# Optimization experiments

Hardware: AMD Instinct MI355X
Metric: run time of the kernel (lower is better)

The kernel has to match this reference:

```python
import jax, jax.numpy as jnp
import numpy as np

EMB_D, N_SLOTS, KEY_D, N_ITER = 768, 8, 128, 5
ATTN_EPS = 1e-8
LN_EPS = 1e-5


def layer_norm(x, g, b):
    mu = jnp.mean(x, axis=-1, keepdims=True)
    var = jnp.mean(jnp.square(x - mu), axis=-1, keepdims=True)
    return (x - mu) * jax.lax.rsqrt(var + LN_EPS) * g + b


def xavier(key, shape):
    fan_in, fan_out = shape[-1], shape[-2] if len(shape) > 1 else shape[-1]
    a = float(np.sqrt(6.0 / (fan_in + fan_out)))
    return jax.random.uniform(key, shape, jnp.float32, -a, a)


def setup_inputs() -> dict:
    key = jax.random.key(0)
    ks = jax.random.split(key, 24)
    B, N = 128, 196
    k = KEY_D
    inp = {
        "features": jax.random.normal(ks[0], (B, N, EMB_D), jnp.float32),
        "slot_noise": jax.random.normal(ks[1], (B, N_SLOTS, k), jnp.float32),
        # LayerNorms
        "ln_in_g": jnp.ones((EMB_D,), jnp.float32), "ln_in_b": jnp.zeros((EMB_D,), jnp.float32),
        "ln_slot_g": jnp.ones((k,), jnp.float32), "ln_slot_b": jnp.zeros((k,), jnp.float32),
        "ln_out_g": jnp.ones((k,), jnp.float32), "ln_out_b": jnp.zeros((k,), jnp.float32),
        "ln_dec_g": jnp.ones((k,), jnp.float32), "ln_dec_b": jnp.zeros((k,), jnp.float32),
        # slot prior
        "mu": xavier(ks[2], (1, 1, k)),
        "log_sigma": xavier(ks[3], (1, 1, k)),
        # projections (torch Linear weight layout: [out, in])
        "Wk": xavier(ks[4], (k, EMB_D)),
        "Wq": xavier(ks[5], (k, k)),
        "Wv": xavier(ks[6], (k, EMB_D)),
        # GRUCell
        "W_ih": jax.random.uniform(ks[7], (3 * k, k), jnp.float32, -1.0/np.sqrt(k), 1.0/np.sqrt(k)),
        "W_hh": jax.random.uniform(ks[8], (3 * k, k), jnp.float32, -1.0/np.sqrt(k), 1.0/np.sqrt(k)),
        "b_ih": jnp.zeros((3 * k,), jnp.float32),
        "b_hh": jnp.zeros((3 * k,), jnp.float32),
        # slot MLP
        "mlp_W1": xavier(ks[9], (k, k)), "mlp_b1": jnp.zeros((k,), jnp.float32),
        "mlp_W2": xavier(ks[10], (k, k)), "mlp_b2": jnp.zeros((k,), jnp.float32),
        # decoder
        "dec_W1": xavier(ks[11], (2 * k, k)), "dec_b1": jnp.zeros((2 * k,), jnp.float32),
        "dec_W2": xavier(ks[12], (EMB_D, 2 * k)), "dec_b2": jnp.zeros((EMB_D,), jnp.float32),
        "dec_W3": xavier(ks[13], (EMB_D, EMB_D)), "dec_b3": jnp.zeros((EMB_D,), jnp.float32),
    }
    return inp


def gru_cell(x, h, W_ih, W_hh, b_ih, b_hh):
    gi = x @ W_ih.T + b_ih  # [*, 3k]
    gh = h @ W_hh.T + b_hh
    ir, iz, inn = jnp.split(gi, 3, axis=-1)
    hr, hz, hn = jnp.split(gh, 3, axis=-1)
    r = jax.nn.sigmoid(ir + hr)
    z = jax.nn.sigmoid(iz + hz)
    n = jnp.tanh(inn + r * hn)
    return (1.0 - z) * n + z * h


def reference(features, slot_noise, ln_in_g, ln_in_b, ln_slot_g, ln_slot_b,
              ln_out_g, ln_out_b, ln_dec_g, ln_dec_b, mu, log_sigma,
              Wk, Wq, Wv, W_ih, W_hh, b_ih, b_hh,
              mlp_W1, mlp_b1, mlp_W2, mlp_b2,
              dec_W1, dec_b1, dec_W2, dec_b2, dec_W3, dec_b3):
    feats_ln = layer_norm(features, ln_in_g, ln_in_b)  # [B,N,E]
    slots = slot_noise * jnp.exp(log_sigma) + mu       # [B,K,D]
    k_proj = (feats_ln @ Wk.T) * (KEY_D ** -0.5)       # [B,N,D]
    v_proj = feats_ln @ Wv.T                           # [B,N,D]

    attn_vis = None
    for _ in range(N_ITER):
        slots_prev = slots
        s_ln = layer_norm(slots, ln_slot_g, ln_slot_b)
        q = s_ln @ Wq.T                                # [B,K,D]
        logits = jnp.einsum('bnd,bkd->bnk', k_proj, q)
        attn_vis = jax.nn.softmax(logits, axis=-1)     # softmax over slots
        attn = attn_vis + ATTN_EPS
        attn = attn / jnp.sum(attn, axis=-2, keepdims=True)  # normalize over tokens
        updates = jnp.einsum('bnk,bnd->bkd', attn, v_proj)
        slots = gru_cell(updates, slots_prev, W_ih, W_hh, b_ih, b_hh)
        h = jax.nn.relu(layer_norm(slots, ln_out_g, ln_out_b) @ mlp_W1.T + mlp_b1)
        slots = slots + (h @ mlp_W2.T + mlp_b2)

    sf = layer_norm(slots, ln_dec_g, ln_dec_b)
    sf = jax.nn.relu(sf @ dec_W1.T + dec_b1)
    sf = jax.nn.relu(sf @ dec_W2.T + dec_b2)
    sf = sf @ dec_W3.T + dec_b3                        # [B,K,E]
    recon = jnp.einsum('bkd,bnk->bnd', sf, attn_vis)   # [B,N,E]
    recon_loss = jnp.mean(jnp.square(recon - features))
    return slots, attn_vis, recon_loss
```

## Files before the change

kernel.cpp:

```cpp
#include <hip/hip_runtime.h>
#include <hip/hip_bf16.h>
#include <math.h>

#define B_    128
#define N_    196
#define E_    768
#define K_    8
#define D_    128
#define BNR   (B_*N_)
#define ITERS 5

#define OFF_PART   0
#define OFF_SDEC   512
#define OFF_WBF    66048
#define OFF_KPBF   639488
#define OFF_VPTBF  2343424
#define OFF_ABF    4178432

typedef __attribute__((ext_vector_type(8))) short bf16x8;
typedef __attribute__((ext_vector_type(4))) float f32x4;

#define MFMA16(a, b, c) __builtin_amdgcn_mfma_f32_16x16x32_bf16(a, b, c, 0, 0, 0)

__device__ __forceinline__ float wave_red_sum64(float v) {
    #pragma unroll
    for (int o = 32; o > 0; o >>= 1) v += __shfl_xor(v, o);
    return v;
}

__device__ __forceinline__ unsigned short f2bf(float v) {
    union { float f; unsigned int u; } c; c.f = v;
    unsigned int u = c.u + 0x7fffu + ((c.u >> 16) & 1u);
    return (unsigned short)(u >> 16);
}

__device__ __forceinline__ void gl_lds16(const void* g, void* l) {
    __builtin_amdgcn_global_load_lds(
        (const __attribute__((address_space(1))) unsigned int*)g,
        (__attribute__((address_space(3))) unsigned int*)l, 16, 0, 0);
}

__device__ __forceinline__ int swz128(int row, int j) {
    return row * 128 + ((((j >> 3) ^ (row & 7))) << 3) + (j & 7);
}
__device__ __forceinline__ int swz256(int row, int j) {
    return row * 256 + ((((j >> 3) ^ (row & 7))) << 3) + (j & 7);
}
__device__ __forceinline__ bf16x8 ldA128(const unsigned short* base, int row, int kq, int ks) {
    int ch = (ks * 4 + kq) ^ (row & 7);
    return *(const bf16x8*)(base + row * 128 + ch * 8);
}
__device__ __forceinline__ bf16x8 ldA256(const unsigned short* base, int row, int kq, int ks) {
    int ch = (ks * 4 + kq) ^ (row & 7);
    return *(const bf16x8*)(base + row * 256 + ch * 8);
}
__device__ __forceinline__ bf16x8 ldW128(const unsigned short* W, int row, int ks, int kq) {
    return *(const bf16x8*)(W + (size_t)row * 128 + ks * 32 + kq * 8);
}

__global__ __launch_bounds__(256) void wfold_k(const float* __restrict__ Wq,
                                               const float* __restrict__ Wk,
                                               unsigned short* __restrict__ WMt) {
    __shared__ __align__(16) unsigned short Aq[128 * 128];
    __shared__ __align__(16) unsigned short Bk[128 * 128];
    const float s = 0.08838834764831845f;
    int t = threadIdx.x;
    int e0 = blockIdx.x * 128;
    for (int idx = t; idx < 16384; idx += 256) {
        int o = idx >> 7, c = idx & 127;
        Aq[swz128(c, o)] = f2bf(Wq[(size_t)o * 128 + c]);
        Bk[swz128(c, o)] = f2bf(Wk[(size_t)o * 768 + e0 + c] * s);
    }
    __syncthreads();
    int w = t >> 6, l = t & 63;
    int wr = w >> 1, wc = w & 1, fr = l & 15, kq = l >> 4;
    f32x4 acc[4][4];
    #pragma unroll
    for (int mi = 0; mi < 4; ++mi)
        #pragma unroll
        for (int nj = 0; nj < 4; ++nj) acc[mi][nj] = (f32x4){0.f, 0.f, 0.f, 0.f};
    #pragma unroll
    for (int ks = 0; ks < 4; ++ks) {
        bf16x8 af[4], bfr[4];
        #pragma unroll
        for (int mi = 0; mi < 4; ++mi) af[mi] = ldA128(Aq, wr * 64 + mi * 16 + fr, kq, ks);
        #pragma unroll
        for (int nj = 0; nj < 4; ++nj) bfr[nj] = ldA128(Bk, wc * 64 + nj * 16 + fr, kq, ks);
        #pragma unroll
        for (int mi = 0; mi < 4; ++mi)
            #pragma unroll
            for (int nj = 0; nj < 4; ++nj)
                acc[mi][nj] = MFMA16(af[mi], bfr[nj], acc[mi][nj]);
    }
    #pragma unroll
    for (int mi = 0; mi < 4; ++mi) {
        int rowbase = wr * 64 + mi * 16 + kq * 4;
        #pragma unroll
        for (int nj = 0; nj < 4; ++nj) {
            int col = e0 + wc * 64 + nj * 16 + fr;
            #pragma unroll
            for (int r = 0; r < 4; ++r)
                WMt[(size_t)(rowbase + r) * 768 + col] = f2bf(acc[mi][nj][r]);
        }
    }
}

struct WCEnt { const float* s; unsigned short* d; int t0; };
struct WCArgs { WCEnt m[8]; };

__global__ __launch_bounds__(256) void wprep_k(WCArgs a,
                                               unsigned short* __restrict__ kpb,
                                               unsigned short* __restrict__ vpt) {
    int bid = blockIdx.x;
    if (bid < 512) {
        int i = 0;
        #pragma unroll
        for (int j = 1; j < 8; ++j) if (bid >= a.m[j].t0) i = j;
        int off = (bid - a.m[i].t0) * 2048 + threadIdx.x * 8;
        const float* s = a.m[i].s + off;
        unsigned short* d = a.m[i].d + off;
        float4 v0 = *(const float4*)s, v1 = *(const float4*)(s + 4);
        ushort4 o0, o1;
        o0.x = f2bf(v0.x); o0.y = f2bf(v0.y); o0.z = f2bf(v0.z); o0.w = f2bf(v0.w);
        o1.x = f2bf(v1.x); o1.y = f2bf(v1.y); o1.z = f2bf(v1.z); o1.w = f2bf(v1.w);
        *(ushort4*)d = o0; *(ushort4*)(d + 4) = o1;
    } else {
        int i = (bid - 512) * 256 + threadIdx.x;
        ushort4 z = {0, 0, 0, 0};
        if (i < 49152) {
            int q = i * 4;
            int b = q / 1536, off = q - b * 1536;
            *(ushort4*)(kpb + ((size_t)b * 208 + 196) * 128 + off) = z;
        } else {
            int c = i - 49152;
            int bd = c / 7, cc = c - bd * 7;
            *(ushort4*)(vpt + (size_t)bd * 224 + 196 + cc * 4) = z;
        }
    }
}

__global__ __launch_bounds__(256) void ln_bf16_k(const float* __restrict__ f,
                                                 const float* __restrict__ g,
                                                 const float* __restrict__ bv,
                                                 unsigned short* __restrict__ out) {
    int wid = blockIdx.x * 4 + (threadIdx.x >> 6);
    int lane = threadIdx.x & 63;
    const float* row = f + (size_t)wid * E_;
    float4 x[3];
    float s = 0.f, s2 = 0.f;
    #pragma unroll
    for (int c = 0; c < 3; ++c) {
        x[c] = *(const float4*)(row + c * 256 + lane * 4);
        s  += x[c].x + x[c].y + x[c].z + x[c].w;
        s2 += x[c].x * x[c].x + x[c].y * x[c].y + x[c].z * x[c].z + x[c].w * x[c].w;
    }
    s  = wave_red_sum64(s);
    s2 = wave_red_sum64(s2);
    float m = s * (1.f / E_);
    float rs = rsqrtf(s2 * (1.f / E_) - m * m + 1e-5f);
    #pragma unroll
    for (int c = 0; c < 3; ++c) {
        float4 g4 = *(const float4*)(g + c * 256 + lane * 4);
        float4 b4 = *(const float4*)(bv + c * 256 + lane * 4);
        ushort4 o;
        o.x = f2bf((x[c].x - m) * rs * g4.x + b4.x);
        o.y = f2bf((x[c].y - m) * rs * g4.y + b4.y);
        o.z = f2bf((x[c].z - m) * rs * g4.z + b4.z);
        o.w = f2bf((x[c].w - m) * rs * g4.w + b4.w);
        *(ushort4*)(out + (size_t)wid * E_ + c * 256 + lane * 4) = o;
    }
}

__global__ __launch_bounds__(256) void mfma_proj_k(const unsigned short* __restrict__ Abf,
                                                   const unsigned short* __restrict__ WMt,
                                                   const unsigned short* __restrict__ Wv_bf,
                                                   unsigned short* __restrict__ kpq_bf,
                                                   unsigned short* __restrict__ vpT_bf) {
    __shared__ __align__(16) unsigned short As[128 * 64];
    __shared__ __align__(16) unsigned short Bs[128 * 64];
    const int t = threadIdx.x, w = t >> 6, l = t & 63;
    const int m0 = blockIdx.x * 128;
    const unsigned short* Wbase = (blockIdx.y == 0) ? WMt : Wv_bf;
    const int wr = w >> 1, wc = w & 1;
    const int fr = l & 15, kq = l >> 4;
    f32x4 acc[4][4];
    #pragma unroll
    for (int mi = 0; mi < 4; ++mi)
        #pragma unroll
        for (int nj = 0; nj < 4; ++nj) acc[mi][nj] = (f32x4){0.f, 0.f, 0.f, 0.f};

    for (int ks = 0; ks < E_; ks += 64) {
        __syncthreads();
        #pragma unroll
        for (int j = 0; j < 4; ++j) {
            int ci = (w << 8) + (j << 6) + l;
            int r = ci >> 3, c = ci & 7;
            int cg = c ^ (r & 7);
            gl_lds16(Abf   + (size_t)(m0 + r) * E_ + ks + cg * 8,
                     As + (size_t)((w << 8) + (j << 6)) * 8);
            gl_lds16(Wbase + (size_t)r * E_ + ks + cg * 8,
                     Bs + (size_t)((w << 8) + (j << 6)) * 8);
        }
        __syncthreads();
        #pragma unroll
        for (int kk = 0; kk < 2; ++kk) {
            bf16x8 af[4], bfr[4];
            int ch = (kk * 4 + kq) ^ (fr & 7);
            #pragma unroll
            for (int mi = 0; mi < 4; ++mi)
                af[mi] = *(const bf16x8*)(As + (wr * 64 + mi * 16 + fr) * 64 + ch * 8);
            #pragma unroll
            for (int nj = 0; nj < 4; ++nj)
                bfr[nj] = *(const bf16x8*)(Bs + (wc * 64 + nj * 16 + fr) * 64 + ch * 8);
            #pragma unroll
            for (int mi = 0; mi < 4; ++mi)
                #pragma unroll
                for (int nj = 0; nj < 4; ++nj)
                    acc[mi][nj] = MFMA16(af[mi], bfr[nj], acc[mi][nj]);
        }
    }
    if (blockIdx.y == 0) {
        #pragma unroll
        for (int mi = 0; mi < 4; ++mi) {
            int rowbase = m0 + wr * 64 + mi * 16 + kq * 4;
            #pragma unroll
            for (int r = 0; r < 4; ++r) {
                int m = rowbase + r;
                int b = m / 196, rr = m - b * 196;
                size_t o = ((size_t)b * 208 + rr) * 128;
                #pragma unroll
                for (int nj = 0; nj < 4; ++nj)
                    kpq_bf[o + wc * 64 + nj * 16 + fr] = f2bf(acc[mi][nj][r]);
            }
        }
    } else {
        #pragma unroll
        for (int mi = 0; mi < 4; ++mi) {
            int rowbase = m0 + wr * 64 + mi * 16 + kq * 4;
            #pragma unroll
            for (int r = 0; r < 4; ++r) {
                int m = rowbase + r;
                int b = m / 196, rr = m - b * 196;
                #pragma unroll
                for (int nj = 0; nj < 4; ++nj) {
                    int col = wc * 64 + nj * 16 + fr;
                    vpT_bf[((size_t)b * 128 + col) * 224 + rr] = f2bf(acc[mi][nj][r]);
                }
            }
        }
    }
}

template<int KTOT, int EPI>
__global__ __launch_bounds__(256) void mfma_mlp_k(const unsigned short* __restrict__ A,
                                                  const unsigned short* __restrict__ Bw,
                                                  const float* __restrict__ bias,
                                                  unsigned short* __restrict__ out_bf,
                                                  float* __restrict__ out_f,
                                                  int ldN) {
    __shared__ __align__(16) unsigned short As[128 * 64];
    __shared__ __align__(16) unsigned short Bs[128 * 64];
    const int t = threadIdx.x, w = t >> 6, l = t & 63;
    const int m0 = blockIdx.x * 128;
    const int n0 = blockIdx.y * 128;
    const int wr = w >> 1, wc = w & 1;
    const int fr = l & 15, kq = l >> 4;
    f32x4 acc[4][4];
    #pragma unroll
    for (int mi = 0; mi < 4; ++mi)
        #pragma unroll
        for (int nj = 0; nj < 4; ++nj) acc[mi][nj] = (f32x4){0.f, 0.f, 0.f, 0.f};

    for (int ks = 0; ks < KTOT; ks += 64) {
        __syncthreads();
        #pragma unroll
        for (int j = 0; j < 4; ++j) {
            int ci = (w << 8) + (j << 6) + l;
            int r = ci >> 3, c = ci & 7;
            int cg = c ^ (r & 7);
            gl_lds16(A  + (size_t)(m0 + r) * KTOT + ks + cg * 8,
                     As + (size_t)((w << 8) + (j << 6)) * 8);
            gl_lds16(Bw + (size_t)(n0 + r) * KTOT + ks + cg * 8,
                     Bs + (size_t)((w << 8) + (j << 6)) * 8);
        }
        __syncthreads();
        #pragma unroll
        for (int kk = 0; kk < 2; ++kk) {
            bf16x8 af[4], bfr[4];
            int ch = (kk * 4 + kq) ^ (fr & 7);
            #pragma unroll
            for (int mi = 0; mi < 4; ++mi)
                af[mi] = *(const bf16x8*)(As + (wr * 64 + mi * 16 + fr) * 64 + ch * 8);
            #pragma unroll
            for (int nj = 0; nj < 4; ++nj)
                bfr[nj] = *(const bf16x8*)(Bs + (wc * 64 + nj * 16 + fr) * 64 + ch * 8);
            #pragma unroll
            for (int mi = 0; mi < 4; ++mi)
                #pragma unroll
                for (int nj = 0; nj < 4; ++nj)
                    acc[mi][nj] = MFMA16(af[mi], bfr[nj], acc[mi][nj]);
        }
    }
    #pragma unroll
    for (int mi = 0; mi < 4; ++mi) {
        int rowbase = m0 + wr * 64 + mi * 16 + kq * 4;
        #pragma unroll
        for (int nj = 0; nj < 4; ++nj) {
            int col = n0 + wc * 64 + nj * 16 + fr;
            float bc = bias[col];
            #pragma unroll
            for (int r = 0; r < 4; ++r) {
                float v = acc[mi][nj][r] + bc;
                if (EPI == 0)
                    out_bf[(size_t)(rowbase + r) * ldN + col] = f2bf(fmaxf(v, 0.f));
                else
                    out_f[(size_t)(rowbase + r) * ldN + col] = v;
            }
        }
    }
}

__global__ __launch_bounds__(512) void slot_iter_mfma(
    const float* __restrict__ noise,
    const float* __restrict__ lsg, const float* __restrict__ lsb,
    const float* __restrict__ log_, const float* __restrict__ lob,
    const float* __restrict__ ldg_, const float* __restrict__ ldb_,
    const float* __restrict__ mup, const float* __restrict__ lsig,
    const unsigned short* __restrict__ Wih_bf,
    const unsigned short* __restrict__ Whh_bf,
    const float* __restrict__ bih, const float* __restrict__ bhh,
    const unsigned short* __restrict__ W1_bf, const float* __restrict__ mb1,
    const unsigned short* __restrict__ W2_bf, const float* __restrict__ mb2,
    const unsigned short* __restrict__ kpq_bf,
    const unsigned short* __restrict__ vpT_bf,
    float* __restrict__ out_slots, float* __restrict__ out_attn,
    unsigned short* __restrict__ sdec_bf) {

    __shared__ float slots[8][128];
    __shared__ float attn[208][9];
    __shared__ float colpart[8][8];
    __shared__ __align__(16) unsigned short sln_bf[2048];
    __shared__ __align__(16) unsigned short upd_bf[2048];
    __shared__ __align__(16) unsigned short slots_bf[2048];
    __shared__ __align__(16) unsigned short h_bf[2048];
    __shared__ __align__(16) unsigned short attnT_bf[4096];

    const int b = blockIdx.x, t = threadIdx.x;
    const int lane = t & 63, w = t >> 6;
    const int fr = lane & 15, kq = lane >> 4;

    for (int i = t; i < 2048; i += 512) {
        sln_bf[i] = 0; upd_bf[i] = 0; slots_bf[i] = 0; h_bf[i] = 0;
    }
    for (int i = t; i < 4096; i += 512) attnT_bf[i] = 0;

    for (int idx = t; idx < 1024; idx += 512) {
        int k = idx >> 7, d = idx & 127;
        float v = noise[(size_t)b * 1024 + idx] * expf(lsig[d]) + mup[d];
        slots[k][d] = v;
        slots_bf[swz128(k, d)] = f2bf(v);
    }
    __syncthreads();

    for (int it = 0; it < ITERS; ++it) {
        bool last = (it == ITERS - 1);
        {
            float x0 = slots[w][lane], x1 = slots[w][lane + 64];
            float s  = wave_red_sum64(x0 + x1);
            float s2 = wave_red_sum64(x0 * x0 + x1 * x1);
            float m = s * 0.0078125f;
            float rs = rsqrtf(s2 * 0.0078125f - m * m + 1e-5f);
            sln_bf[swz128(w, lane)]      = f2bf((x0 - m) * rs * lsg[lane]      + lsb[lane]);
            sln_bf[swz128(w, lane + 64)] = f2bf((x1 - m) * rs * lsg[lane + 64] + lsb[lane + 64]);
        }
        __syncthreads();
        {
            float cp = 0.f;
            #pragma unroll
            for (int p = 0; p < 2; ++p) {
                int tt = w + p * 8;
                if (tt <= 12) {
                    f32x4 acc = {0.f, 0.f, 0.f, 0.f};
                    const unsigned short* kpr = kpq_bf + ((size_t)b * 208 + tt * 16 + fr) * 128;
                    #pragma unroll
                    for (int ks = 0; ks < 4; ++ks)
                        acc = MFMA16(*(const bf16x8*)(kpr + ks * 32 + kq * 8),
                                     ldA128(sln_bf, fr, kq, ks), acc);
                    #pragma unroll
                    for (int r = 0; r < 4; ++r) {
                        float v = acc[r];
                        float mx = fmaxf(v, __shfl_xor(v, 1));
                        mx = fmaxf(mx, __shfl_xor(mx, 2));
                        mx = fmaxf(mx, __shfl_xor(mx, 4));
                        float e = expf(v - mx);
                        float sm = e;
                        sm += __shfl_xor(sm, 1); sm += __shfl_xor(sm, 2); sm += __shfl_xor(sm, 4);
                        float a = e / sm;
                        int tok = tt * 16 + kq * 4 + r;
                        bool valid = (tok < 196);
                        if (fr < 8 && valid) attn[tok][fr] = a;
                        cp += valid ? a : 0.f;
                    }
                }
            }
            cp += __shfl_xor(cp, 16);
            cp += __shfl_xor(cp, 32);
            if (lane < 8) colpart[w][lane] = cp;
        }
        __syncthreads();
        {
            int k = t & 7;
            float cs = colpart[0][k] + colpart[1][k] + colpart[2][k] + colpart[3][k]
                     + colpart[4][k] + colpart[5][k] + colpart[6][k] + colpart[7][k]
                     + 196.0f * 1e-8f;
            float inv = 1.f / cs;
            for (int idx = t; idx < 1568; idx += 512) {
                int n = idx >> 3;
                float raw = attn[n][k];
                attnT_bf[swz256(k, n)] = f2bf((raw + 1e-8f) * inv);
                if (last) out_attn[((size_t)b * 196 + n) * 8 + k] = raw;
            }
        }
        __syncthreads();
        {
            f32x4 acc = {0.f, 0.f, 0.f, 0.f};
            const unsigned short* vpr = vpT_bf + ((size_t)b * 128 + w * 16 + fr) * 224;
            #pragma unroll
            for (int ks = 0; ks < 7; ++ks)
                acc = MFMA16(ldA256(attnT_bf, fr, kq, ks),
                             *(const bf16x8*)(vpr + ks * 32 + kq * 8), acc);
            if (kq < 2) {
                #pragma unroll
                for (int r = 0; r < 4; ++r)
                    upd_bf[swz128(kq * 4 + r, w * 16 + fr)] = f2bf(acc[r]);
            }
        }
        __syncthreads();
        {
            f32x4 gi0 = {0,0,0,0}, gi1 = {0,0,0,0}, gi2 = {0,0,0,0};
            f32x4 gh0 = {0,0,0,0}, gh1 = {0,0,0,0}, gh2 = {0,0,0,0};
            #pragma unroll
            for (int ks = 0; ks < 4; ++ks) {
                bf16x8 au = ldA128(upd_bf,   fr, kq, ks);
                bf16x8 as = ldA128(slots_bf, fr, kq, ks);
                gi0 = MFMA16(au, ldW128(Wih_bf,       w * 16 + fr, ks, kq), gi0);
                gi1 = MFMA16(au, ldW128(Wih_bf, 128 + w * 16 + fr, ks, kq), gi1);
                gi2 = MFMA16(au, ldW128(Wih_bf, 256 + w * 16 + fr, ks, kq), gi2);
                gh0 = MFMA16(as, ldW128(Whh_bf,       w * 16 + fr, ks, kq), gh0);
                gh1 = MFMA16(as, ldW128(Whh_bf, 128 + w * 16 + fr, ks, kq), gh1);
                gh2 = MFMA16(as, ldW128(Whh_bf, 256 + w * 16 + fr, ks, kq), gh2);
            }
            if (kq < 2) {
                int d = w * 16 + fr;
                float bi0 = bih[d], bi1 = bih[128 + d], bi2 = bih[256 + d];
                float bh0 = bhh[d], bh1 = bhh[128 + d], bh2 = bhh[256 + d];
                #pragma unroll
                for (int r = 0; r < 4; ++r) {
                    int m = kq * 4 + r;
                    float rr = 1.f / (1.f + expf(-((gi0[r] + bi0) + (gh0[r] + bh0))));
                    float zz = 1.f / (1.f + expf(-((gi1[r] + bi1) + (gh1[r] + bh1))));
                    float nn = tanhf((gi2[r] + bi2) + rr * (gh2[r] + bh2));
                    float h = slots[m][d];
                    slots[m][d] = (1.f - zz) * nn + zz * h;
                }
            }
        }
        __syncthreads();
        {
            float x0 = slots[w][lane], x1 = slots[w][lane + 64];
            float s  = wave_red_sum64(x0 + x1);
            float s2 = wave_red_sum64(x0 * x0 + x1 * x1);
            float m = s * 0.0078125f;
            float rs = rsqrtf(s2 * 0.0078125f - m * m + 1e-5f);
            sln_bf[swz128(w, lane)]      = f2bf((x0 - m) * rs * log_[lane]      + lob[lane]);
            sln_bf[swz128(w, lane + 64)] = f2bf((x1 - m) * rs * log_[lane + 64] + lob[lane + 64]);
        }
        __syncthreads();
        {
            f32x4 acc = {0.f, 0.f, 0.f, 0.f};
            #pragma unroll
            for (int ks = 0; ks < 4; ++ks)
                acc = MFMA16(ldA128(sln_bf, fr, kq, ks), ldW128(W1_bf, w * 16 + fr, ks, kq), acc);
            if (kq < 2) {
                float b1 = mb1[w * 16 + fr];
                #pragma unroll
                for (int r = 0; r < 4; ++r)
                    h_bf[swz128(kq * 4 + r, w * 16 + fr)] = f2bf(fmaxf(acc[r] + b1, 0.f));
            }
        }
        __syncthreads();
        {
            f32x4 acc = {0.f, 0.f, 0.f, 0.f};
            #pragma unroll
            for (int ks = 0; ks < 4; ++ks)
                acc = MFMA16(ldA128(h_bf, fr, kq, ks), ldW128(W2_bf, w * 16 + fr, ks, kq), acc);
            if (kq < 2) {
                float b2 = mb2[w * 16 + fr];
                #pragma unroll
                for (int r = 0; r < 4; ++r) {
                    int m = kq * 4 + r, d = w * 16 + fr;
                    float v = slots[m][d] + acc[r] + b2;
                    slots[m][d] = v;
                    slots_bf[swz128(m, d)] = f2bf(v);
                }
            }
        }
        __syncthreads();
    }
    {
        float x0 = slots[w][lane], x1 = slots[w][lane + 64];
        out_slots[(size_t)b * 1024 + w * 128 + lane]      = x0;
        out_slots[(size_t)b * 1024 + w * 128 + lane + 64] = x1;
        float s  = wave_red_sum64(x0 + x1);
        float s2 = wave_red_sum64(x0 * x0 + x1 * x1);
        float m = s * 0.0078125f;
        float rs = rsqrtf(s2 * 0.0078125f - m * m + 1e-5f);
        sdec_bf[((size_t)b * 8 + w) * 128 + lane]      = f2bf((x0 - m) * rs * ldg_[lane]      + ldb_[lane]);
        sdec_bf[((size_t)b * 8 + w) * 128 + lane + 64] = f2bf((x1 - m) * rs * ldg_[lane + 64] + ldb_[lane + 64]);
    }
}

__global__ __launch_bounds__(256) void recon_loss_k(
    const float* __restrict__ feats, const float* __restrict__ attnv,
    const float* __restrict__ sf, float* __restrict__ partials) {

    __shared__ float sfl[8][768];
    __shared__ float al[49][8];
    __shared__ float wred[4];
    int b = blockIdx.x, qd = blockIdx.y, t = threadIdx.x;
    for (int idx = t; idx < 8 * 768; idx += 256)
        ((float*)sfl)[idx] = sf[(size_t)b * 8 * 768 + idx];
    int n0 = qd * 49;
    for (int idx = t; idx < 49 * 8; idx += 256)
        ((float*)al)[idx] = attnv[((size_t)b * N_ + n0) * 8 + idx];
    __syncthreads();
    float acc = 0.f;
    for (int nl = 0; nl < 49; ++nl) {
        float a0 = al[nl][0], a1 = al[nl][1], a2 = al[nl][2], a3 = al[nl][3];
        float a4 = al[nl][4], a5 = al[nl][5], a6 = al[nl][6], a7 = al[nl][7];
        const float* frow = feats + ((size_t)(b * N_ + n0 + nl)) * E_;
        for (int c = t; c < E_; c += 256) {
            float r = sfl[0][c]*a0 + sfl[1][c]*a1 + sfl[2][c]*a2 + sfl[3][c]*a3
                    + sfl[4][c]*a4 + sfl[5][c]*a5 + sfl[6][c]*a6 + sfl[7][c]*a7;
            float d = r - frow[c];
            acc += d * d;
        }
    }
    acc = wave_red_sum64(acc);
    int lane = t & 63, w = t >> 6;
    if (lane == 0) wred[w] = acc;
    __syncthreads();
    if (t == 0) partials[b * 4 + qd] = wred[0] + wred[1] + wred[2] + wred[3];
}

__global__ __launch_bounds__(512) void loss_final_k(const float* __restrict__ partials,
                                                    float* __restrict__ out) {
    __shared__ float wred[8];
    int t = threadIdx.x;
    float v = partials[t];
    v = wave_red_sum64(v);
    if ((t & 63) == 0) wred[t >> 6] = v;
    __syncthreads();
    if (t == 0) {
        float s = 0.f;
        #pragma unroll
        for (int i = 0; i < 8; ++i) s += wred[i];
        out[0] = s / (float)(B_ * N_ * E_);
    }
}

extern "C" void kernel_launch(void* const* d_in, const int* in_sizes, int n_in,
                              void* d_out, int out_size, void* d_ws, size_t ws_size,
                              hipStream_t stream) {
    (void)in_sizes; (void)n_in; (void)out_size; (void)ws_size;
    const float* feats     = (const float*)d_in[0];
    const float* noise     = (const float*)d_in[1];
    const float* ln_in_g   = (const float*)d_in[2];
    const float* ln_in_b   = (const float*)d_in[3];
    const float* ln_slot_g = (const float*)d_in[4];
    const float* ln_slot_b = (const float*)d_in[5];
    const float* ln_out_g  = (const float*)d_in[6];
    const float* ln_out_b  = (const float*)d_in[7];
    const float* ln_dec_g  = (const float*)d_in[8];
    const float* ln_dec_b  = (const float*)d_in[9];
    const float* mu        = (const float*)d_in[10];
    const float* log_sigma = (const float*)d_in[11];
    const float* Wk        = (const float*)d_in[12];
    const float* Wq        = (const float*)d_in[13];
    const float* Wv        = (const float*)d_in[14];
    const float* W_ih      = (const float*)d_in[15];
    const float* W_hh      = (const float*)d_in[16];
    const float* b_ih      = (const float*)d_in[17];
    const float* b_hh      = (const float*)d_in[18];
    const float* mlp_W1    = (const float*)d_in[19];
    const float* mlp_b1    = (const float*)d_in[20];
    const float* mlp_W2    = (const float*)d_in[21];
    const float* mlp_b2    = (const float*)d_in[22];
    const float* dec_W1    = (const float*)d_in[23];
    const float* dec_b1    = (const float*)d_in[24];
    const float* dec_W2    = (const float*)d_in[25];
    const float* dec_b2    = (const float*)d_in[26];
    const float* dec_W3    = (const float*)d_in[27];
    const float* dec_b3    = (const float*)d_in[28];

    float* ws    = (float*)d_ws;
    float* parts = ws + OFF_PART;
    unsigned short* sdec_bf = (unsigned short*)(ws + OFF_SDEC);
    unsigned short* Wbase   = (unsigned short*)(ws + OFF_WBF);
    unsigned short* Wv_bf   = Wbase;
    unsigned short* Wih_bf  = Wbase + 98304;
    unsigned short* Whh_bf  = Wbase + 147456;
    unsigned short* W1_bf   = Wbase + 196608;
    unsigned short* W2_bf   = Wbase + 212992;
    unsigned short* dW1_bf  = Wbase + 229376;
    unsigned short* dW2_bf  = Wbase + 262144;
    unsigned short* dW3_bf  = Wbase + 458752;
    unsigned short* WMt     = Wbase + 1048576;
    unsigned short* kpq_bf  = (unsigned short*)(ws + OFF_KPBF);
    unsigned short* vpT_bf  = (unsigned short*)(ws + OFF_VPTBF);
    unsigned short* Abf     = (unsigned short*)(ws + OFF_ABF);
    float*          sf      = ws + OFF_ABF;
    unsigned short* h1_bf   = (unsigned short*)(ws + OFF_ABF + 786432);
    unsigned short* h2_bf   = (unsigned short*)(ws + OFF_ABF + 786432 + 131072);

    float* out_slots = (float*)d_out;
    float* out_attn  = out_slots + 131072;
    float* out_loss  = out_slots + 331776;

    wfold_k<<<6, 256, 0, stream>>>(Wq, Wk, WMt);

    WCArgs wa;
    wa.m[0] = {Wv,     Wv_bf,  0};
    wa.m[1] = {W_ih,   Wih_bf, 48};
    wa.m[2] = {W_hh,   Whh_bf, 72};
    wa.m[3] = {mlp_W1, W1_bf,  96};
    wa.m[4] = {mlp_W2, W2_bf,  104};
    wa.m[5] = {dec_W1, dW1_bf, 112};
    wa.m[6] = {dec_W2, dW2_bf, 128};
    wa.m[7] = {dec_W3, dW3_bf, 224};
    wprep_k<<<1152, 256, 0, stream>>>(wa, kpq_bf, vpT_bf);

    ln_bf16_k<<<BNR / 4, 256, 0, stream>>>(feats, ln_in_g, ln_in_b, Abf);
    mfma_proj_k<<<dim3(BNR / 128, 2), 256, 0, stream>>>(Abf, WMt, Wv_bf, kpq_bf, vpT_bf);

    slot_iter_mfma<<<B_, 512, 0, stream>>>(noise, ln_slot_g, ln_slot_b, ln_out_g, ln_out_b,
                                           ln_dec_g, ln_dec_b, mu, log_sigma,
                                           Wih_bf, Whh_bf, b_ih, b_hh,
                                           W1_bf, mlp_b1, W2_bf, mlp_b2, kpq_bf, vpT_bf,
                                           out_slots, out_attn, sdec_bf);

    mfma_mlp_k<128, 0><<<dim3(8, 2), 256, 0, stream>>>(sdec_bf, dW1_bf, dec_b1, h1_bf, nullptr, 256);
    mfma_mlp_k<256, 0><<<dim3(8, 6), 256, 0, stream>>>(h1_bf,  dW2_bf, dec_b2, h2_bf, nullptr, 768);
    mfma_mlp_k<768, 1><<<dim3(8, 6), 256, 0, stream>>>(h2_bf,  dW3_bf, dec_b3, nullptr, sf, 768);

    recon_loss_k<<<dim3(B_, 4), 256, 0, stream>>>(feats, out_attn, sf, parts);
    loss_final_k<<<1, 512, 0, stream>>>(parts, out_loss);
}
```

Measured before the change: 200.9 us.

## Fuse decoder MLP into slot kernel and merge K/V projections into one block

The three decoder GEMM launches are removed, and the decoder MLP (dec_W1, dec_W2, dec_W3 with ReLU) now runs at the end of the per-batch slot kernel using MFMA, with intermediates kept in LDS. The projection kernel now computes both the folded key projection and the value projection in one 512-thread block that shares the A tile. The transposed value output is staged through LDS so it can be written with vector stores. This saves three launches, halves reads of the normalized features, and replaces scattered 2-byte transposed stores. In exchange the slot kernel uses more LDS and does a 768-wide GEMM on only 8 rows per block, which underuses the MFMA tiles.

```diff
diff --git a/kernel.cpp b/kernel.cpp
--- a/kernel.cpp
+++ b/kernel.cpp
@@ -11,7 +11,6 @@
 #define ITERS 5
 
 #define OFF_PART   0
-#define OFF_SDEC   512
 #define OFF_WBF    66048
 #define OFF_KPBF   639488
 #define OFF_VPTBF  2343424
@@ -46,6 +45,9 @@
 __device__ __forceinline__ int swz256(int row, int j) {
     return row * 256 + ((((j >> 3) ^ (row & 7))) << 3) + (j & 7);
 }
+__device__ __forceinline__ int swz768(int row, int j) {
+    return row * 768 + ((((j >> 3) ^ (row & 7))) << 3) + (j & 7);
+}
 __device__ __forceinline__ bf16x8 ldA128(const unsigned short* base, int row, int kq, int ks) {
     int ch = (ks * 4 + kq) ^ (row & 7);
     return *(const bf16x8*)(base + row * 128 + ch * 8);
@@ -53,6 +55,10 @@
 __device__ __forceinline__ bf16x8 ldA256(const unsigned short* base, int row, int kq, int ks) {
     int ch = (ks * 4 + kq) ^ (row & 7);
     return *(const bf16x8*)(base + row * 256 + ch * 8);
+}
+__device__ __forceinline__ bf16x8 ldA768(const unsigned short* base, int row, int kq, int ks) {
+    int ch = (ks * 4 + kq) ^ (row & 7);
+    return *(const bf16x8*)(base + row * 768 + ch * 8);
 }
 __device__ __forceinline__ bf16x8 ldW128(const unsigned short* W, int row, int ks, int kq) {
     return *(const bf16x8*)(W + (size_t)row * 128 + ks * 32 + kq * 8);
@@ -171,17 +177,16 @@
     }
 }
 
-__global__ __launch_bounds__(256) void mfma_proj_k(const unsigned short* __restrict__ Abf,
+__global__ __launch_bounds__(512) void mfma_proj_k(const unsigned short* __restrict__ Abf,
                                                    const unsigned short* __restrict__ WMt,
                                                    const unsigned short* __restrict__ Wv_bf,
                                                    unsigned short* __restrict__ kpq_bf,
                                                    unsigned short* __restrict__ vpT_bf) {
     __shared__ __align__(16) unsigned short As[128 * 64];
-    __shared__ __align__(16) unsigned short Bs[128 * 64];
+    __shared__ __align__(16) unsigned short Bs[256 * 64];
     const int t = threadIdx.x, w = t >> 6, l = t & 63;
     const int m0 = blockIdx.x * 128;
-    const unsigned short* Wbase = (blockIdx.y == 0) ? WMt : Wv_bf;
-    const int wr = w >> 1, wc = w & 1;
+    const int wr = w >> 2, wc = w & 3;
     const int fr = l & 15, kq = l >> 4;
     f32x4 acc[4][4];
     #pragma unroll
@@ -192,26 +197,35 @@
     for (int ks = 0; ks < E_; ks += 64) {
         __syncthreads();
         #pragma unroll
+        for (int j = 0; j < 2; ++j) {
+            int ci = j * 512 + (w << 6) + l;
+            int r = ci >> 3, c = ci & 7, cg = c ^ (r & 7);
+            gl_lds16(Abf + (size_t)(m0 + r) * E_ + ks + cg * 8,
+                     As + (size_t)(j * 512 + (w << 6)) * 8);
+        }
+        #pragma unroll
         for (int j = 0; j < 4; ++j) {
-            int ci = (w << 8) + (j << 6) + l;
-            int r = ci >> 3, c = ci & 7;
-            int cg = c ^ (r & 7);
-            gl_lds16(Abf   + (size_t)(m0 + r) * E_ + ks + cg * 8,
-                     As + (size_t)((w << 8) + (j << 6)) * 8);
-            gl_lds16(Wbase + (size_t)r * E_ + ks + cg * 8,
-                     Bs + (size_t)((w << 8) + (j << 6)) * 8);
+            int ci = j * 512 + (w << 6) + l;
+            int r = ci >> 3, c = ci & 7, cg = c ^ (r & 7);
+            const unsigned short* src = (r < 128)
+                ? WMt   + (size_t)r * E_ + ks + cg * 8
+                : Wv_bf + (size_t)(r - 128) * E_ + ks + cg * 8;
+            gl_lds16(src, Bs + (size_t)(j * 512 + (w << 6)) * 8);
         }
         __syncthreads();
         #pragma unroll
         for (int kk = 0; kk < 2; ++kk) {
             bf16x8 af[4], bfr[4];
-            int ch = (kk * 4 + kq) ^ (fr & 7);
-            #pragma unroll
-            for (int mi = 0; mi < 4; ++mi)
-                af[mi] = *(const bf16x8*)(As + (wr * 64 + mi * 16 + fr) * 64 + ch * 8);
-            #pragma unroll
-            for (int nj = 0; nj < 4; ++nj)
-                bfr[nj] = *(const bf16x8*)(Bs + (wc * 64 + nj * 16 + fr) * 64 + ch * 8);
+            #pragma unroll
+            for (int mi = 0; mi < 4; ++mi) {
+                int rr = wr * 64 + mi * 16 + fr;
+                af[mi] = *(const bf16x8*)(As + rr * 64 + (((kk * 4 + kq) ^ (rr & 7))) * 8);
+            }
+            #pragma unroll
+            for (int nj = 0; nj < 4; ++nj) {
+                int rr = wc * 64 + nj * 16 + fr;
+                bfr[nj] = *(const bf16x8*)(Bs + rr * 64 + (((kk * 4 + kq) ^ (rr & 7))) * 8);
+            }
             #pragma unroll
             for (int mi = 0; mi < 4; ++mi)
                 #pragma unroll
@@ -219,7 +233,8 @@
                     acc[mi][nj] = MFMA16(af[mi], bfr[nj], acc[mi][nj]);
         }
     }
-    if (blockIdx.y == 0) {
+    __syncthreads();
+    if (wc < 2) {
         #pragma unroll
         for (int mi = 0; mi < 4; ++mi) {
             int rowbase = m0 + wr * 64 + mi * 16 + kq * 4;
@@ -234,87 +249,42 @@
             }
         }
     } else {
+        int dbase = (wc - 2) * 64;
         #pragma unroll
         for (int mi = 0; mi < 4; ++mi) {
-            int rowbase = m0 + wr * 64 + mi * 16 + kq * 4;
-            #pragma unroll
-            for (int r = 0; r < 4; ++r) {
-                int m = rowbase + r;
-                int b = m / 196, rr = m - b * 196;
+            int tok = wr * 64 + mi * 16 + kq * 4;
+            #pragma unroll
+            for (int nj = 0; nj < 4; ++nj) {
+                int d = dbase + nj * 16 + fr;
+                ushort4 pk;
+                pk.x = f2bf(acc[mi][nj][0]); pk.y = f2bf(acc[mi][nj][1]);
+                pk.z = f2bf(acc[mi][nj][2]); pk.w = f2bf(acc[mi][nj][3]);
+                *(ushort4*)(Bs + d * 128 + (tok ^ ((d & 7) << 3))) = pk;
+            }
+        }
+    }
+    __syncthreads();
+    {
+        int d = t >> 2, mg = t & 3;
+        #pragma unroll
+        for (int sc = 0; sc < 4; ++sc) {
+            int mstart = mg * 32 + sc * 8;
+            int cm = mstart >> 3;
+            const unsigned short* src = Bs + d * 128 + ((cm ^ (d & 7)) << 3);
+            int g0 = m0 + mstart;
+            int b0 = g0 / 196, rr0 = g0 - b0 * 196;
+            int b7 = (g0 + 7) / 196;
+            if (b0 == b7) {
+                unsigned short* dst = vpT_bf + ((size_t)b0 * 128 + d) * 224 + rr0;
+                *(ushort4*)(dst)     = *(const ushort4*)(src);
+                *(ushort4*)(dst + 4) = *(const ushort4*)(src + 4);
+            } else {
                 #pragma unroll
-                for (int nj = 0; nj < 4; ++nj) {
-                    int col = wc * 64 + nj * 16 + fr;
-                    vpT_bf[((size_t)b * 128 + col) * 224 + rr] = f2bf(acc[mi][nj][r]);
+                for (int e = 0; e < 8; ++e) {
+                    int g = g0 + e;
+                    int bb = g / 196, rr = g - bb * 196;
+                    vpT_bf[((size_t)bb * 128 + d) * 224 + rr] = src[e];
                 }
-            }
-        }
-    }
-}
-
-template<int KTOT, int EPI>
-__global__ __launch_bounds__(256) void mfma_mlp_k(const unsigned short* __restrict__ A,
-                                                  const unsigned short* __restrict__ Bw,
-                                                  const float* __restrict__ bias,
-                                                  unsigned short* __restrict__ out_bf,
-                                                  float* __restrict__ out_f,
-                                                  int ldN) {
-    __shared__ __align__(16) unsigned short As[128 * 64];
-    __shared__ __align__(16) unsigned short Bs[128 * 64];
-    const int t = threadIdx.x, w = t >> 6, l = t & 63;
-    const int m0 = blockIdx.x * 128;
-    const int n0 = blockIdx.y * 128;
-    const int wr = w >> 1, wc = w & 1;
-    const int fr = l & 15, kq = l >> 4;
-    f32x4 acc[4][4];
-    #pragma unroll
-    for (int mi = 0; mi < 4; ++mi)
-        #pragma unroll
-        for (int nj = 0; nj < 4; ++nj) acc[mi][nj] = (f32x4){0.f, 0.f, 0.f, 0.f};
-
-    for (int ks = 0; ks < KTOT; ks += 64) {
-        __syncthreads();
-        #pragma unroll
-        for (int j = 0; j < 4; ++j) {
-            int ci = (w << 8) + (j << 6) + l;
-            int r = ci >> 3, c = ci & 7;
-            int cg = c ^ (r & 7);
-            gl_lds16(A  + (size_t)(m0 + r) * KTOT + ks + cg * 8,
-                     As + (size_t)((w << 8) + (j << 6)) * 8);
-            gl_lds16(Bw + (size_t)(n0 + r) * KTOT + ks + cg * 8,
-                     Bs + (size_t)((w << 8) + (j << 6)) * 8);
-        }
-        __syncthreads();
-        #pragma unroll
-        for (int kk = 0; kk < 2; ++kk) {
-            bf16x8 af[4], bfr[4];
-            int ch = (kk * 4 + kq) ^ (fr & 7);
-            #pragma unroll
-            for (int mi = 0; mi < 4; ++mi)
-                af[mi] = *(const bf16x8*)(As + (wr * 64 + mi * 16 + fr) * 64 + ch * 8);
-            #pragma unroll
-            for (int nj = 0; nj < 4; ++nj)
-                bfr[nj] = *(const bf16x8*)(Bs + (wc * 64 + nj * 16 + fr) * 64 + ch * 8);
-            #pragma unroll
-            for (int mi = 0; mi < 4; ++mi)
-                #pragma unroll
-                for (int nj = 0; nj < 4; ++nj)
-                    acc[mi][nj] = MFMA16(af[mi], bfr[nj], acc[mi][nj]);
-        }
-    }
-    #pragma unroll
-    for (int mi = 0; mi < 4; ++mi) {
-        int rowbase = m0 + wr * 64 + mi * 16 + kq * 4;
-        #pragma unroll
-        for (int nj = 0; nj < 4; ++nj) {
-            int col = n0 + wc * 64 + nj * 16 + fr;
-            float bc = bias[col];
-            #pragma unroll
-            for (int r = 0; r < 4; ++r) {
-                float v = acc[mi][nj][r] + bc;
-                if (EPI == 0)
-                    out_bf[(size_t)(rowbase + r) * ldN + col] = f2bf(fmaxf(v, 0.f));
-                else
-                    out_f[(size_t)(rowbase + r) * ldN + col] = v;
             }
         }
     }
@@ -333,8 +303,11 @@
     const unsigned short* __restrict__ W2_bf, const float* __restrict__ mb2,
     const unsigned short* __restrict__ kpq_bf,
     const unsigned short* __restrict__ vpT_bf,
+    const unsigned short* __restrict__ dW1, const float* __restrict__ db1,
+    const unsigned short* __restrict__ dW2, const float* __restrict__ db2,
+    const unsigned short* __restrict__ dW3, const float* __restrict__ db3,
     float* __restrict__ out_slots, float* __restrict__ out_attn,
-    unsigned short* __restrict__ sdec_bf) {
+    float* __restrict__ sf) {
 
     __shared__ float slots[8][128];
     __shared__ float attn[208][9];
@@ -344,6 +317,7 @@
     __shared__ __align__(16) unsigned short slots_bf[2048];
     __shared__ __align__(16) unsigned short h_bf[2048];
     __shared__ __align__(16) unsigned short attnT_bf[4096];
+    __shared__ __align__(16) unsigned short h2_lds[12288];
 
     const int b = blockIdx.x, t = threadIdx.x;
     const int lane = t & 63, w = t >> 6;
@@ -353,6 +327,7 @@
         sln_bf[i] = 0; upd_bf[i] = 0; slots_bf[i] = 0; h_bf[i] = 0;
     }
     for (int i = t; i < 4096; i += 512) attnT_bf[i] = 0;
+    for (int i = t; i < 12288; i += 512) h2_lds[i] = 0;
 
     for (int idx = t; idx < 1024; idx += 512) {
         int k = idx >> 7, d = idx & 127;
@@ -515,8 +490,56 @@
         float s2 = wave_red_sum64(x0 * x0 + x1 * x1);
         float m = s * 0.0078125f;
         float rs = rsqrtf(s2 * 0.0078125f - m * m + 1e-5f);
-        sdec_bf[((size_t)b * 8 + w) * 128 + lane]      = f2bf((x0 - m) * rs * ldg_[lane]      + ldb_[lane]);
-        sdec_bf[((size_t)b * 8 + w) * 128 + lane + 64] = f2bf((x1 - m) * rs * ldg_[lane + 64] + ldb_[lane + 64]);
+        sln_bf[swz128(w, lane)]      = f2bf((x0 - m) * rs * ldg_[lane]      + ldb_[lane]);
+        sln_bf[swz128(w, lane + 64)] = f2bf((x1 - m) * rs * ldg_[lane + 64] + ldb_[lane + 64]);
+    }
+    __syncthreads();
+    #pragma unroll
+    for (int p = 0; p < 2; ++p) {
+        int nt = w + p * 8;
+        f32x4 acc = {0.f, 0.f, 0.f, 0.f};
+        #pragma unroll
+        for (int ks = 0; ks < 4; ++ks)
+            acc = MFMA16(ldA128(sln_bf, fr, kq, ks),
+                         *(const bf16x8*)(dW1 + (size_t)(nt * 16 + fr) * 128 + ks * 32 + kq * 8), acc);
+        if (kq < 2) {
+            float bb = db1[nt * 16 + fr];
+            #pragma unroll
+            for (int r = 0; r < 4; ++r)
+                attnT_bf[swz256(kq * 4 + r, nt * 16 + fr)] = f2bf(fmaxf(acc[r] + bb, 0.f));
+        }
+    }
+    __syncthreads();
+    #pragma unroll
+    for (int p = 0; p < 6; ++p) {
+        int nt = p * 8 + w;
+        f32x4 acc = {0.f, 0.f, 0.f, 0.f};
+        #pragma unroll
+        for (int ks = 0; ks < 8; ++ks)
+            acc = MFMA16(ldA256(attnT_bf, fr, kq, ks),
+                         *(const bf16x8*)(dW2 + (size_t)(nt * 16 + fr) * 256 + ks * 32 + kq * 8), acc);
+        if (kq < 2) {
+            float bb = db2[nt * 16 + fr];
+            #pragma unroll
+            for (int r = 0; r < 4; ++r)
+                h2_lds[swz768(kq * 4 + r, nt * 16 + fr)] = f2bf(fmaxf(acc[r] + bb, 0.f));
+        }
+    }
+    __syncthreads();
+    #pragma unroll
+    for (int p = 0; p < 6; ++p) {
+        int nt = p * 8 + w;
+        f32x4 acc = {0.f, 0.f, 0.f, 0.f};
+        #pragma unroll
+        for (int ks = 0; ks < 24; ++ks)
+            acc = MFMA16(ldA768(h2_lds, fr, kq, ks),
+                         *(const bf16x8*)(dW3 + (size_t)(nt * 16 + fr) * 768 + ks * 32 + kq * 8), acc);
+        if (kq < 2) {
+            float bb = db3[nt * 16 + fr];
+            #pragma unroll
+            for (int r = 0; r < 4; ++r)
+                sf[((size_t)b * 8 + kq * 4 + r) * 768 + nt * 16 + fr] = acc[r] + bb;
+        }
     }
 }
 
@@ -605,7 +628,6 @@
 
     float* ws    = (float*)d_ws;
     float* parts = ws + OFF_PART;
-    unsigned short* sdec_bf = (unsigned short*)(ws + OFF_SDEC);
     unsigned short* Wbase   = (unsigned short*)(ws + OFF_WBF);
     unsigned short* Wv_bf   = Wbase;
     unsigned short* Wih_bf  = Wbase + 98304;
@@ -620,8 +642,6 @@
     unsigned short* vpT_bf  = (unsigned short*)(ws + OFF_VPTBF);
     unsigned short* Abf     = (unsigned short*)(ws + OFF_ABF);
     float*          sf      = ws + OFF_ABF;
-    unsigned short* h1_bf   = (unsigned short*)(ws + OFF_ABF + 786432);
-    unsigned short* h2_bf   = (unsigned short*)(ws + OFF_ABF + 786432 + 131072);
 
     float* out_slots = (float*)d_out;
     float* out_attn  = out_slots + 131072;
@@ -641,17 +661,14 @@
     wprep_k<<<1152, 256, 0, stream>>>(wa, kpq_bf, vpT_bf);
 
     ln_bf16_k<<<BNR / 4, 256, 0, stream>>>(feats, ln_in_g, ln_in_b, Abf);
-    mfma_proj_k<<<dim3(BNR / 128, 2), 256, 0, stream>>>(Abf, WMt, Wv_bf, kpq_bf, vpT_bf);
+    mfma_proj_k<<<BNR / 128, 512, 0, stream>>>(Abf, WMt, Wv_bf, kpq_bf, vpT_bf);
 
     slot_iter_mfma<<<B_, 512, 0, stream>>>(noise, ln_slot_g, ln_slot_b, ln_out_g, ln_out_b,
                                            ln_dec_g, ln_dec_b, mu, log_sigma,
                                            Wih_bf, Whh_bf, b_ih, b_hh,
                                            W1_bf, mlp_b1, W2_bf, mlp_b2, kpq_bf, vpT_bf,
-                                           out_slots, out_attn, sdec_bf);
-
-    mfma_mlp_k<128, 0><<<dim3(8, 2), 256, 0, stream>>>(sdec_bf, dW1_bf, dec_b1, h1_bf, nullptr, 256);
-    mfma_mlp_k<256, 0><<<dim3(8, 6), 256, 0, stream>>>(h1_bf,  dW2_bf, dec_b2, h2_bf, nullptr, 768);
-    mfma_mlp_k<768, 1><<<dim3(8, 6), 256, 0, stream>>>(h2_bf,  dW3_bf, dec_b3, nullptr, sf, 768);
+                                           dW1_bf, dec_b1, dW2_bf, dec_b2, dW3_bf, dec_b3,
+                                           out_slots, out_attn, sf);
 
     recon_loss_k<<<dim3(B_, 4), 256, 0, stream>>>(feats, out_attn, sf, parts);
     loss_final_k<<<1, 512, 0, stream>>>(parts, out_loss);
```

Result: slower. 226.8 us (+12.9%).

## Fuse K and V projections into one 512-thread block with LDS-staged transposed V store

Applied to the files above, without the earlier changes.

The projection kernel now computes both the folded key projection and the value projection in a single 512-thread block that covers 256 output columns, so each A tile is loaded from global memory once instead of twice. The value half of the accumulator is written into a swizzled LDS buffer (reusing Bs), then stored to the transposed vpT layout as 8-element vector writes instead of scattered 2-byte stores. This adds LDS footprint and an extra synchronisation, and halves the grid size, which may lower occupancy.

```diff
diff --git a/kernel.cpp b/kernel.cpp
--- a/kernel.cpp
+++ b/kernel.cpp
@@ -171,17 +171,16 @@
     }
 }
 
-__global__ __launch_bounds__(256) void mfma_proj_k(const unsigned short* __restrict__ Abf,
+__global__ __launch_bounds__(512) void mfma_proj_k(const unsigned short* __restrict__ Abf,
                                                    const unsigned short* __restrict__ WMt,
                                                    const unsigned short* __restrict__ Wv_bf,
                                                    unsigned short* __restrict__ kpq_bf,
                                                    unsigned short* __restrict__ vpT_bf) {
     __shared__ __align__(16) unsigned short As[128 * 64];
-    __shared__ __align__(16) unsigned short Bs[128 * 64];
+    __shared__ __align__(16) unsigned short Bs[256 * 64];
     const int t = threadIdx.x, w = t >> 6, l = t & 63;
     const int m0 = blockIdx.x * 128;
-    const unsigned short* Wbase = (blockIdx.y == 0) ? WMt : Wv_bf;
-    const int wr = w >> 1, wc = w & 1;
+    const int wr = w >> 2, wc = w & 3;
     const int fr = l & 15, kq = l >> 4;
     f32x4 acc[4][4];
     #pragma unroll
@@ -192,26 +191,35 @@
     for (int ks = 0; ks < E_; ks += 64) {
         __syncthreads();
         #pragma unroll
+        for (int j = 0; j < 2; ++j) {
+            int ci = j * 512 + (w << 6) + l;
+            int r = ci >> 3, c = ci & 7, cg = c ^ (r & 7);
+            gl_lds16(Abf + (size_t)(m0 + r) * E_ + ks + cg * 8,
+                     As + (size_t)(j * 512 + (w << 6)) * 8);
+        }
+        #pragma unroll
         for (int j = 0; j < 4; ++j) {
-            int ci = (w << 8) + (j << 6) + l;
-            int r = ci >> 3, c = ci & 7;
-            int cg = c ^ (r & 7);
-            gl_lds16(Abf   + (size_t)(m0 + r) * E_ + ks + cg * 8,
-                     As + (size_t)((w << 8) + (j << 6)) * 8);
-            gl_lds16(Wbase + (size_t)r * E_ + ks + cg * 8,
-                     Bs + (size_t)((w << 8) + (j << 6)) * 8);
+            int ci = j * 512 + (w << 6) + l;
+            int r = ci >> 3, c = ci & 7, cg = c ^ (r & 7);
+            const unsigned short* src = (r < 128)
+                ? WMt   + (size_t)r * E_ + ks + cg * 8
+                : Wv_bf + (size_t)(r - 128) * E_ + ks + cg * 8;
+            gl_lds16(src, Bs + (size_t)(j * 512 + (w << 6)) * 8);
         }
         __syncthreads();
         #pragma unroll
         for (int kk = 0; kk < 2; ++kk) {
             bf16x8 af[4], bfr[4];
-            int ch = (kk * 4 + kq) ^ (fr & 7);
-            #pragma unroll
-            for (int mi = 0; mi < 4; ++mi)
-                af[mi] = *(const bf16x8*)(As + (wr * 64 + mi * 16 + fr) * 64 + ch * 8);
-            #pragma unroll
-            for (int nj = 0; nj < 4; ++nj)
-                bfr[nj] = *(const bf16x8*)(Bs + (wc * 64 + nj * 16 + fr) * 64 + ch * 8);
+            #pragma unroll
+            for (int mi = 0; mi < 4; ++mi) {
+                int rr = wr * 64 + mi * 16 + fr;
+                af[mi] = *(const bf16x8*)(As + rr * 64 + (((kk * 4 + kq) ^ (rr & 7))) * 8);
+            }
+            #pragma unroll
+            for (int nj = 0; nj < 4; ++nj) {
+                int rr = wc * 64 + nj * 16 + fr;
+                bfr[nj] = *(const bf16x8*)(Bs + rr * 64 + (((kk * 4 + kq) ^ (rr & 7))) * 8);
+            }
             #pragma unroll
             for (int mi = 0; mi < 4; ++mi)
                 #pragma unroll
@@ -219,7 +227,8 @@
                     acc[mi][nj] = MFMA16(af[mi], bfr[nj], acc[mi][nj]);
         }
     }
-    if (blockIdx.y == 0) {
+    __syncthreads();
+    if (wc < 2) {
         #pragma unroll
         for (int mi = 0; mi < 4; ++mi) {
             int rowbase = m0 + wr * 64 + mi * 16 + kq * 4;
@@ -234,17 +243,41 @@
             }
         }
     } else {
+        int dbase = (wc - 2) * 64;
         #pragma unroll
         for (int mi = 0; mi < 4; ++mi) {
-            int rowbase = m0 + wr * 64 + mi * 16 + kq * 4;
-            #pragma unroll
-            for (int r = 0; r < 4; ++r) {
-                int m = rowbase + r;
-                int b = m / 196, rr = m - b * 196;
-                #pragma unroll
-                for (int nj = 0; nj < 4; ++nj) {
-                    int col = wc * 64 + nj * 16 + fr;
-                    vpT_bf[((size_t)b * 128 + col) * 224 + rr] = f2bf(acc[mi][nj][r]);
+            int tok = wr * 64 + mi * 16 + kq * 4;
+            #pragma unroll
+            for (int nj = 0; nj < 4; ++nj) {
+                int d = dbase + nj * 16 + fr;
+                ushort4 pk;
+                pk.x = f2bf(acc[mi][nj][0]); pk.y = f2bf(acc[mi][nj][1]);
+                pk.z = f2bf(acc[mi][nj][2]); pk.w = f2bf(acc[mi][nj][3]);
+                *(ushort4*)(Bs + d * 128 + (tok ^ ((d & 7) << 3))) = pk;
+            }
+        }
+    }
+    __syncthreads();
+    {
+        int d = t >> 2, mg = t & 3;
+        #pragma unroll
+        for (int sc = 0; sc < 4; ++sc) {
+            int mstart = mg * 32 + sc * 8;
+            int cm = mstart >> 3;
+            const unsigned short* src = Bs + d * 128 + ((cm ^ (d & 7)) << 3);
+            int g0 = m0 + mstart;
+            int b0 = g0 / 196, rr0 = g0 - b0 * 196;
+            int b7 = (g0 + 7) / 196;
+            if (b0 == b7) {
+                unsigned short* dst = vpT_bf + ((size_t)b0 * 128 + d) * 224 + rr0;
+                *(ushort4*)(dst)     = *(const ushort4*)(src);
+                *(ushort4*)(dst + 4) = *(const ushort4*)(src + 4);
+            } else {
+                #pragma unroll
+                for (int e = 0; e < 8; ++e) {
+                    int g = g0 + e;
+                    int bb = g / 196, rr = g - bb * 196;
+                    vpT_bf[((size_t)bb * 128 + d) * 224 + rr] = src[e];
                 }
             }
         }
@@ -641,7 +674,7 @@
     wprep_k<<<1152, 256, 0, stream>>>(wa, kpq_bf, vpT_bf);
 
     ln_bf16_k<<<BNR / 4, 256, 0, stream>>>(feats, ln_in_g, ln_in_b, Abf);
-    mfma_proj_k<<<dim3(BNR / 128, 2), 256, 0, stream>>>(Abf, WMt, Wv_bf, kpq_bf, vpT_bf);
+    mfma_proj_k<<<BNR / 128, 512, 0, stream>>>(Abf, WMt, Wv_bf, kpq_bf, vpT_bf);
 
     slot_iter_mfma<<<B_, 512, 0, stream>>>(noise, ln_slot_g, ln_slot_b, ln_out_g, ln_out_b,
                                            ln_dec_g, ln_dec_b, mu, log_sigma,
```

Result: no change. 199.2 us (median of 2 runs) (-0.9%).
